# Kernel optimization log

Hardware: AMD Instinct MI355X
Metric: run time of the kernel (lower is better)

The kernel has to match this reference:

```python
import jax, jax.numpy as jnp
import numpy as np

T, B, D = 4096, 8, 256  # tgt_len, batch, embed dim
P, O = 256, 256         # proj_dim, out_dim


def setup_inputs() -> dict:
    key = jax.random.key(0)
    k1, k2, k3, k4, k5 = jax.random.split(key, 5)
    return {
        "query": jax.random.normal(k1, (T, B, D), dtype=jnp.float32),
        "W_kqv": jax.random.normal(k2, (D, 3 * P), dtype=jnp.float32) * (D ** -0.5),
        "b_kqv": jax.random.normal(k3, (3 * P,), dtype=jnp.float32) * 0.02,
        "W_out": jax.random.normal(k4, (P, O), dtype=jnp.float32) * (P ** -0.5),
        "b_out": jax.random.normal(k5, (O,), dtype=jnp.float32) * 0.02,
    }


def reference(query, W_kqv, b_kqv, W_out, b_out):
    # query: [T, B, D] (Time x Batch x Channel)
    p = W_kqv.shape[1] // 3
    scaling = p ** -0.5
    qkv = query @ W_kqv + b_kqv                      # [T, B, 3P]
    q, k, v = jnp.split(qkv, 3, axis=-1)             # each [T, B, P]
    q = (q * scaling).transpose(1, 0, 2)             # [B, T, P]
    k = k.transpose(1, 0, 2)                         # [B, S, P] (S == T)
    v = v.transpose(1, 0, 2)                         # [B, S, P]
    scores = jnp.einsum('btp,bsp->bts', q, k)        # [B, T, S]
    probs = jax.nn.softmax(scores.astype(jnp.float32), axis=-1).astype(q.dtype)
    attn = jnp.einsum('bts,bsp->btp', probs, v)      # [B, T, P]
    attn = attn.transpose(1, 0, 2)                   # [T, B, P]
    return attn @ W_out + b_out                      # [T, B, O]
```

## Files before the change

### kernel.cpp

```cpp
#include <hip/hip_runtime.h>
#include <hip/hip_bf16.h>

#define T_LEN 4096
#define BATCH 8
#define D_DIM 256
#define P_DIM 256
#define O_DIM 256
#define N3    768

typedef __bf16 bf16;
typedef __attribute__((ext_vector_type(8))) __bf16 bf16x8;
typedef __attribute__((ext_vector_type(4))) __bf16 bf16x4;
typedef __attribute__((ext_vector_type(4))) float f32x4;
typedef __attribute__((ext_vector_type(16))) float f32x16;

#define MFMA16(a, b, c) __builtin_amdgcn_mfma_f32_16x16x32_bf16(a, b, c, 0, 0, 0)
#define MFMA32(a, b, c) __builtin_amdgcn_mfma_f32_32x32x16_bf16(a, b, c, 0, 0, 0)

#define LDS_P 72

#define BARRIER_LGKM() __asm__ __volatile__("s_waitcnt lgkmcnt(0)\n\ts_barrier" ::: "memory")

__global__ __launch_bounds__(256) void wpack_kernel(
    const float* __restrict__ src, bf16* __restrict__ dst, int ncols)
{
    const int g = blockIdx.x * 256 + threadIdx.x;
    const int lane = g & 63;
    const int idx = g >> 6;
    const int nt = idx & 3, kt = (idx >> 2) & 7, ch = idx >> 5;
    const int n = ch * 64 + nt * 16 + (lane & 15);
    const int kb = kt * 32 + (lane >> 4) * 8;
    bf16x8 pk;
    #pragma unroll
    for (int j = 0; j < 8; ++j) pk[j] = (bf16)src[(size_t)(kb + j) * ncols + n];
    *(bf16x8*)&dst[(size_t)g * 8] = pk;
}

__global__ __launch_bounds__(256) void qkv_proj_kernel(
    const float* __restrict__ query, const bf16* __restrict__ wkp,
    const float* __restrict__ b_kqv,
    bf16* __restrict__ qb, bf16* __restrict__ kpk, bf16* __restrict__ vpk)
{
    __shared__ __align__(16) bf16 Vt[64][68];
    const int m0 = blockIdx.x * 64;
    const int tid = threadIdx.x;
    const int lane = tid & 63, wave = tid >> 6, l15 = lane & 15, quad = lane >> 4;
    const int arow = wave * 16 + l15;

    bf16x8 af[8];
    {
        const float* qsrc = query + (size_t)(m0 + arow) * D_DIM + quad * 8;
        #pragma unroll
        for (int kt = 0; kt < 8; ++kt) {
            float4 f0 = *(const float4*)(qsrc + kt * 32);
            float4 f1 = *(const float4*)(qsrc + kt * 32 + 4);
            af[kt] = bf16x8{(bf16)f0.x, (bf16)f0.y, (bf16)f0.z, (bf16)f0.w,
                            (bf16)f1.x, (bf16)f1.y, (bf16)f1.z, (bf16)f1.w};
        }
    }

    for (int ch = 0; ch < 12; ++ch) {
        f32x4 acc[4];
        #pragma unroll
        for (int i = 0; i < 4; ++i)
            for (int r = 0; r < 4; ++r) acc[i][r] = 0.f;
        #pragma unroll
        for (int kt = 0; kt < 8; ++kt) {
            #pragma unroll
            for (int nt = 0; nt < 4; ++nt) {
                bf16x8 bb = *(const bf16x8*)&wkp[((((size_t)ch * 8 + kt) * 4 + nt) * 64 + lane) * 8];
                acc[nt] = MFMA16(af[kt], bb, acc[nt]);
            }
        }
        if (ch < 4) {
            #pragma unroll
            for (int nt = 0; nt < 4; ++nt) {
                const int c = ch * 64 + nt * 16 + l15;
                const float bias = b_kqv[c];
                #pragma unroll
                for (int r = 0; r < 4; ++r) {
                    const int m = m0 + wave * 16 + quad * 4 + r;
                    const int t = m >> 3, bi = m & 7;
                    qb[((size_t)bi * T_LEN + t) * P_DIM + c] = (bf16)((acc[nt][r] + bias) * 0.0625f);
                }
            }
        } else if (ch < 8) {
            #pragma unroll
            for (int nt = 0; nt < 4; ++nt) {
                const int c = ch * 64 + nt * 16 + l15;
                const float bias = b_kqv[c];
                const int kk = c - 256;
                const int c16 = kk >> 4, halfk = (kk >> 3) & 1, j = kk & 7;
                #pragma unroll
                for (int r = 0; r < 4; ++r) {
                    const int m = m0 + wave * 16 + quad * 4 + r;
                    const int t = m >> 3, bi = m & 7;
                    const int st32 = t >> 5, n31 = t & 31;
                    kpk[((((size_t)bi * 128 + st32) * 16 + c16) * 64 + halfk * 32 + n31) * 8 + j]
                        = (bf16)(acc[nt][r] + bias);
                }
            }
        } else {
            __syncthreads();
            #pragma unroll
            for (int nt = 0; nt < 4; ++nt) {
                const int c = ch * 64 + nt * 16 + l15;
                const float bias = b_kqv[c];
                #pragma unroll
                for (int r = 0; r < 4; ++r)
                    Vt[nt * 16 + l15][wave * 16 + quad * 4 + r] = (bf16)(acc[nt][r] + bias);
            }
            __syncthreads();
            const int t0g = m0 >> 3;
            const int s64 = t0g >> 6, ks = (t0g >> 4) & 3, halfv = (t0g >> 3) & 1;
            #pragma unroll
            for (int uu = 0; uu < 2; ++uu) {
                const int u = tid * 2 + uu;
                const int cl = u >> 3, bi = u & 7;
                bf16x8 pk;
                #pragma unroll
                for (int j = 0; j < 8; ++j) pk[j] = Vt[cl][j * 8 + bi];
                const int cc = (ch - 8) * 64 + cl;
                const int ptG = cc >> 5, n31 = cc & 31;
                *(bf16x8*)&vpk[((((size_t)bi * 64 + s64) * 4 + ks) * 8 + ptG) * 512
                               + (size_t)(halfv * 32 + n31) * 8] = pk;
            }
        }
    }
}

__global__ __launch_bounds__(256, 2) void flash_attn_kernel(
    const bf16* __restrict__ qb, const bf16* __restrict__ kpk,
    const bf16* __restrict__ vpk, bf16* __restrict__ attn)
{
    __shared__ __align__(16) bf16 Ps[2][64][LDS_P];
    __shared__ float l_red[2][64];

    const int bid = blockIdx.x;
    const int b = bid & 7;
    const int t0 = (bid >> 3) * 64;
    const int tid = threadIdx.x;
    const int lane = tid & 63, wave = tid >> 6;
    const int l31 = lane & 31, half = lane >> 5;
    const int rg = wave & 1, sh = wave >> 1;

    bf16x8 qf[16];
    {
        const bf16* qrow = qb + ((size_t)b * T_LEN + t0 + rg * 32 + l31) * P_DIM + half * 8;
        #pragma unroll
        for (int kt = 0; kt < 16; ++kt) qf[kt] = *(const bf16x8*)(qrow + kt * 16);
    }

    f32x16 acc_o[2][2];
    float l_part[16];
    #pragma unroll
    for (int i = 0; i < 16; ++i) {
        acc_o[0][0][i] = 0.f; acc_o[0][1][i] = 0.f;
        acc_o[1][0][i] = 0.f; acc_o[1][1][i] = 0.f;
        l_part[i] = 0.f;
    }

    const bf16* kfb = kpk + (size_t)b * 128 * 16 * 512;
    const bf16* vfb = vpk + (size_t)b * 64 * 4 * 8 * 512;

    bf16x8 kpre[8];
    {
        const bf16* kf0 = kfb + ((size_t)sh * 16 * 64 + lane) * 8;
        #pragma unroll
        for (int c = 0; c < 8; ++c) kpre[c] = *(const bf16x8*)(kf0 + (size_t)c * 512);
    }

    for (int s0 = 0; s0 < T_LEN; s0 += 64) {
        const int buf = (s0 >> 6) & 1;
        const bf16* kf  = kfb + (((size_t)((s0 >> 5) + sh)) * 16 * 64 + lane) * 8;
        const bf16* kfn = kfb + (((size_t)(((s0 + 64) >> 5) + sh)) * 16 * 64 + lane) * 8;

        bf16x8 kc2[8];
        #pragma unroll
        for (int c = 0; c < 8; ++c) kc2[c] = *(const bf16x8*)(kf + (size_t)(8 + c) * 512);

        f32x16 accs;
        #pragma unroll
        for (int i = 0; i < 16; ++i) accs[i] = 0.f;
        #pragma unroll
        for (int c = 0; c < 8; ++c) accs = MFMA32(qf[c], kpre[c], accs);
        #pragma unroll
        for (int c = 0; c < 8; ++c) accs = MFMA32(qf[8 + c], kc2[c], accs);

        const bf16* vf = vfb + (((size_t)(s0 >> 6) * 4) * 8 + wave * 2) * 512 + (size_t)lane * 8;
        bf16x8 bv[8];
        #pragma unroll
        for (int ks = 0; ks < 4; ++ks) {
            bv[ks * 2]     = *(const bf16x8*)(vf + (size_t)ks * 8 * 512);
            bv[ks * 2 + 1] = *(const bf16x8*)(vf + (size_t)(ks * 8 + 1) * 512);
        }
        #pragma unroll
        for (int c = 0; c < 8; ++c) kpre[c] = *(const bf16x8*)(kfn + (size_t)c * 512);

        #pragma unroll
        for (int r = 0; r < 16; ++r) {
            float p = __expf(accs[r]);
            bf16 pb = (bf16)p;
            l_part[r] += (float)pb;
            int row = rg * 32 + (r & 3) + 8 * (r >> 2) + 4 * half;
            Ps[buf][row][sh * 32 + l31] = pb;
        }

        BARRIER_LGKM();

        #pragma unroll
        for (int ks = 0; ks < 4; ++ks) {
            bf16x8 ap0 = *(const bf16x8*)&Ps[buf][l31][ks * 16 + half * 8];
            bf16x8 ap1 = *(const bf16x8*)&Ps[buf][32 + l31][ks * 16 + half * 8];
            acc_o[0][0] = MFMA32(ap0, bv[ks * 2],     acc_o[0][0]);
            acc_o[0][1] = MFMA32(ap0, bv[ks * 2 + 1], acc_o[0][1]);
            acc_o[1][0] = MFMA32(ap1, bv[ks * 2],     acc_o[1][0]);
            acc_o[1][1] = MFMA32(ap1, bv[ks * 2 + 1], acc_o[1][1]);
        }
    }

    #pragma unroll
    for (int r = 0; r < 16; ++r) {
        float v = l_part[r];
        v += __shfl_xor(v, 1, 64);
        v += __shfl_xor(v, 2, 64);
        v += __shfl_xor(v, 4, 64);
        v += __shfl_xor(v, 8, 64);
        v += __shfl_xor(v, 16, 64);
        l_part[r] = v;
    }
    if (l31 == 0) {
        #pragma unroll
        for (int r = 0; r < 16; ++r) {
            const int row = rg * 32 + (r & 3) + 8 * (r >> 2) + 4 * half;
            l_red[sh][row] = l_part[r];
        }
    }
    __syncthreads();

    #pragma unroll
    for (int rt = 0; rt < 2; ++rt) {
        #pragma unroll
        for (int r = 0; r < 16; ++r) {
            const int row = rt * 32 + (r & 3) + 8 * (r >> 2) + 4 * half;
            const float linv = 1.0f / (l_red[0][row] + l_red[1][row]);
            bf16* dst = attn + ((size_t)(t0 + row) * BATCH + b) * P_DIM + wave * 64 + l31;
            dst[0]  = (bf16)(acc_o[rt][0][r] * linv);
            dst[32] = (bf16)(acc_o[rt][1][r] * linv);
        }
    }
}

__global__ __launch_bounds__(256) void out_proj_kernel(
    const bf16* __restrict__ attn, const bf16* __restrict__ wop,
    const float* __restrict__ b_out, float* __restrict__ out)
{
    const int m0 = blockIdx.x * 64;
    const int tid = threadIdx.x;
    const int lane = tid & 63, wave = tid >> 6, l15 = lane & 15, quad = lane >> 4;
    const int arow = wave * 16 + l15;

    bf16x8 af[8];
    {
        const bf16* asrc = attn + (size_t)(m0 + arow) * P_DIM + quad * 8;
        #pragma unroll
        for (int kt = 0; kt < 8; ++kt) af[kt] = *(const bf16x8*)(asrc + kt * 32);
    }

    for (int ch = 0; ch < 4; ++ch) {
        f32x4 acc[4];
        #pragma unroll
        for (int i = 0; i < 4; ++i)
            for (int r = 0; r < 4; ++r) acc[i][r] = 0.f;
        #pragma unroll
        for (int kt = 0; kt < 8; ++kt) {
            #pragma unroll
            for (int nt = 0; nt < 4; ++nt) {
                bf16x8 bb = *(const bf16x8*)&wop[((((size_t)ch * 8 + kt) * 4 + nt) * 64 + lane) * 8];
                acc[nt] = MFMA16(af[kt], bb, acc[nt]);
            }
        }
        #pragma unroll
        for (int nt = 0; nt < 4; ++nt) {
            const int n = ch * 64 + nt * 16 + l15;
            const float bias = b_out[n];
            #pragma unroll
            for (int r = 0; r < 4; ++r) {
                const int m = m0 + wave * 16 + quad * 4 + r;
                out[(size_t)m * O_DIM + n] = acc[nt][r] + bias;
            }
        }
    }
}

extern "C" void kernel_launch(void* const* d_in, const int* in_sizes, int n_in,
                              void* d_out, int out_size, void* d_ws, size_t ws_size,
                              hipStream_t stream) {
    const float* query = (const float*)d_in[0];
    const float* W_kqv = (const float*)d_in[1];
    const float* b_kqv = (const float*)d_in[2];
    const float* W_out = (const float*)d_in[3];
    const float* b_out = (const float*)d_in[4];
    float* out = (float*)d_out;

    const size_t BUF = (size_t)BATCH * T_LEN * P_DIM;
    bf16* qb   = (bf16*)d_ws;
    bf16* kpk  = qb + BUF;
    bf16* vpk  = kpk + BUF;
    bf16* attn = vpk + BUF;
    bf16* wkp = attn;
    bf16* wop = qb;

    wpack_kernel<<<96, 256, 0, stream>>>(W_kqv, wkp, N3);
    qkv_proj_kernel<<<512, 256, 0, stream>>>(query, wkp, b_kqv, qb, kpk, vpk);
    flash_attn_kernel<<<512, 256, 0, stream>>>(qb, kpk, vpk, attn);
    wpack_kernel<<<32, 256, 0, stream>>>(W_out, wop, O_DIM);
    out_proj_kernel<<<512, 256, 0, stream>>>(attn, wop, b_out, out);
}
```

Before: 283.5 us.

## Software-pipeline attention loop so PV of previous tile overlaps QK of current

Restructures the flash-attention main loop into a two-stage software pipeline. Each iteration computes QK^T and softmax for the current 64-key tile while issuing the PV MFMAs for the previous tile from the other LDS buffer. V fragments are double-buffered in registers (bvA/bvB), and there is a prologue and epilogue. This aims to hide the exp and LDS write latency behind MFMA work and to drop one barrier wait from the critical path, at the cost of more register pressure.

```diff
diff --git a/kernel.cpp b/kernel.cpp
--- a/kernel.cpp
+++ b/kernel.cpp
@@ -170,54 +170,75 @@
         for (int c = 0; c < 8; ++c) kpre[c] = *(const bf16x8*)(kf0 + (size_t)c * 512);
     }
 
-    for (int s0 = 0; s0 < T_LEN; s0 += 64) {
-        const int buf = (s0 >> 6) & 1;
-        const bf16* kf  = kfb + (((size_t)((s0 >> 5) + sh)) * 16 * 64 + lane) * 8;
-        const bf16* kfn = kfb + (((size_t)(((s0 + 64) >> 5) + sh)) * 16 * 64 + lane) * 8;
-
-        bf16x8 kc2[8];
-        #pragma unroll
-        for (int c = 0; c < 8; ++c) kc2[c] = *(const bf16x8*)(kf + (size_t)(8 + c) * 512);
-
-        f32x16 accs;
-        #pragma unroll
-        for (int i = 0; i < 16; ++i) accs[i] = 0.f;
-        #pragma unroll
-        for (int c = 0; c < 8; ++c) accs = MFMA32(qf[c], kpre[c], accs);
-        #pragma unroll
-        for (int c = 0; c < 8; ++c) accs = MFMA32(qf[8 + c], kc2[c], accs);
-
-        const bf16* vf = vfb + (((size_t)(s0 >> 6) * 4) * 8 + wave * 2) * 512 + (size_t)lane * 8;
-        bf16x8 bv[8];
+    bf16x8 bvA[8], bvB[8];
+
+#define FA_ITER(S0, BVP, BVC, DO_PV)                                          \
+{                                                                             \
+    const int buf = ((S0) >> 6) & 1;                                          \
+    const bf16* kf  = kfb + (((size_t)(((S0) >> 5) + sh)) * 16 * 64 + lane) * 8;        \
+    const bf16* kfn = kfb + (((size_t)((((S0) + 64) >> 5) + sh)) * 16 * 64 + lane) * 8; \
+    bf16x8 kc2[8];                                                            \
+    _Pragma("unroll")                                                         \
+    for (int c = 0; c < 8; ++c) kc2[c] = *(const bf16x8*)(kf + (size_t)(8 + c) * 512);  \
+    f32x16 accs;                                                              \
+    _Pragma("unroll")                                                         \
+    for (int i = 0; i < 16; ++i) accs[i] = 0.f;                               \
+    _Pragma("unroll")                                                         \
+    for (int c = 0; c < 8; ++c) accs = MFMA32(qf[c], kpre[c], accs);          \
+    _Pragma("unroll")                                                         \
+    for (int c = 0; c < 8; ++c) accs = MFMA32(qf[8 + c], kc2[c], accs);       \
+    _Pragma("unroll")                                                         \
+    for (int c = 0; c < 8; ++c) kpre[c] = *(const bf16x8*)(kfn + (size_t)c * 512);      \
+    if (DO_PV) {                                                              \
+        const int pbuf = buf ^ 1;                                             \
+        _Pragma("unroll")                                                     \
+        for (int ks = 0; ks < 4; ++ks) {                                      \
+            bf16x8 ap0 = *(const bf16x8*)&Ps[pbuf][l31][ks * 16 + half * 8];  \
+            bf16x8 ap1 = *(const bf16x8*)&Ps[pbuf][32 + l31][ks * 16 + half * 8];       \
+            acc_o[0][0] = MFMA32(ap0, BVP[ks * 2],     acc_o[0][0]);          \
+            acc_o[0][1] = MFMA32(ap0, BVP[ks * 2 + 1], acc_o[0][1]);          \
+            acc_o[1][0] = MFMA32(ap1, BVP[ks * 2],     acc_o[1][0]);          \
+            acc_o[1][1] = MFMA32(ap1, BVP[ks * 2 + 1], acc_o[1][1]);          \
+        }                                                                     \
+    }                                                                         \
+    _Pragma("unroll")                                                         \
+    for (int r = 0; r < 16; ++r) {                                            \
+        float p = __expf(accs[r]);                                            \
+        bf16 pb = (bf16)p;                                                    \
+        l_part[r] += (float)pb;                                               \
+        int row = rg * 32 + (r & 3) + 8 * (r >> 2) + 4 * half;                \
+        Ps[buf][row][sh * 32 + l31] = pb;                                     \
+    }                                                                         \
+    const bf16* vf = vfb + (((size_t)((S0) >> 6) * 4) * 8 + wave * 2) * 512 + (size_t)lane * 8; \
+    _Pragma("unroll")                                                         \
+    for (int ks = 0; ks < 4; ++ks) {                                          \
+        BVC[ks * 2]     = *(const bf16x8*)(vf + (size_t)ks * 8 * 512);        \
+        BVC[ks * 2 + 1] = *(const bf16x8*)(vf + (size_t)(ks * 8 + 1) * 512);  \
+    }                                                                         \
+    BARRIER_LGKM();                                                           \
+}
+
+    FA_ITER(0, bvB, bvA, 0)
+
+    for (int s0 = 64; s0 < 4032; s0 += 128) {
+        FA_ITER(s0,      bvA, bvB, 1)
+        FA_ITER(s0 + 64, bvB, bvA, 1)
+    }
+
+    FA_ITER(4032, bvA, bvB, 1)
+
+    {
         #pragma unroll
         for (int ks = 0; ks < 4; ++ks) {
-            bv[ks * 2]     = *(const bf16x8*)(vf + (size_t)ks * 8 * 512);
-            bv[ks * 2 + 1] = *(const bf16x8*)(vf + (size_t)(ks * 8 + 1) * 512);
-        }
-        #pragma unroll
-        for (int c = 0; c < 8; ++c) kpre[c] = *(const bf16x8*)(kfn + (size_t)c * 512);
-
-        #pragma unroll
-        for (int r = 0; r < 16; ++r) {
-            float p = __expf(accs[r]);
-            bf16 pb = (bf16)p;
-            l_part[r] += (float)pb;
-            int row = rg * 32 + (r & 3) + 8 * (r >> 2) + 4 * half;
-            Ps[buf][row][sh * 32 + l31] = pb;
-        }
-
-        BARRIER_LGKM();
-
-        #pragma unroll
-        for (int ks = 0; ks < 4; ++ks) {
-            bf16x8 ap0 = *(const bf16x8*)&Ps[buf][l31][ks * 16 + half * 8];
-            bf16x8 ap1 = *(const bf16x8*)&Ps[buf][32 + l31][ks * 16 + half * 8];
-            acc_o[0][0] = MFMA32(ap0, bv[ks * 2],     acc_o[0][0]);
-            acc_o[0][1] = MFMA32(ap0, bv[ks * 2 + 1], acc_o[0][1]);
-            acc_o[1][0] = MFMA32(ap1, bv[ks * 2],     acc_o[1][0]);
-            acc_o[1][1] = MFMA32(ap1, bv[ks * 2 + 1], acc_o[1][1]);
-        }
-    }
+            bf16x8 ap0 = *(const bf16x8*)&Ps[1][l31][ks * 16 + half * 8];
+            bf16x8 ap1 = *(const bf16x8*)&Ps[1][32 + l31][ks * 16 + half * 8];
+            acc_o[0][0] = MFMA32(ap0, bvB[ks * 2],     acc_o[0][0]);
+            acc_o[0][1] = MFMA32(ap0, bvB[ks * 2 + 1], acc_o[0][1]);
+            acc_o[1][0] = MFMA32(ap1, bvB[ks * 2],     acc_o[1][0]);
+            acc_o[1][1] = MFMA32(ap1, bvB[ks * 2 + 1], acc_o[1][1]);
+        }
+    }
+#undef FA_ITER
 
     #pragma unroll
     for (int r = 0; r < 16; ++r) {
```

After: 290.2 us. 2.4% more time.

## Enlarge flash-attention tile to 128 query rows with 8 waves per block

Applied to the files above, without the earlier changes.

Each flash-attention block now covers 128 query rows using 512 threads (8 waves) instead of 64 rows with 4 waves. The grid halves to 256 blocks. Each wave computes scores for 32 rows by 32 keys and accumulates a 32-column output slice across all 128 rows. This halves the per-block K/V global traffic relative to the query rows handled and cuts V-fragment registers per wave. In exchange, each block needs more LDS, the barrier spans more waves, and 256 blocks may underfill the CUs on MI355X.

```diff
diff --git a/kernel.cpp b/kernel.cpp
--- a/kernel.cpp
+++ b/kernel.cpp
@@ -129,34 +129,34 @@
     }
 }
 
-__global__ __launch_bounds__(256, 2) void flash_attn_kernel(
+__global__ __launch_bounds__(512, 2) void flash_attn_kernel(
     const bf16* __restrict__ qb, const bf16* __restrict__ kpk,
     const bf16* __restrict__ vpk, bf16* __restrict__ attn)
 {
-    __shared__ __align__(16) bf16 Ps[2][64][LDS_P];
-    __shared__ float l_red[2][64];
+    __shared__ __align__(16) bf16 Ps[2][128][LDS_P];
+    __shared__ float l_red[2][128];
 
     const int bid = blockIdx.x;
     const int b = bid & 7;
-    const int t0 = (bid >> 3) * 64;
+    const int t0 = (bid >> 3) * 128;
     const int tid = threadIdx.x;
     const int lane = tid & 63, wave = tid >> 6;
     const int l31 = lane & 31, half = lane >> 5;
-    const int rg = wave & 1, sh = wave >> 1;
+    const int sh = wave & 1, tg = wave >> 1;
 
     bf16x8 qf[16];
     {
-        const bf16* qrow = qb + ((size_t)b * T_LEN + t0 + rg * 32 + l31) * P_DIM + half * 8;
+        const bf16* qrow = qb + ((size_t)b * T_LEN + t0 + tg * 32 + l31) * P_DIM + half * 8;
         #pragma unroll
         for (int kt = 0; kt < 16; ++kt) qf[kt] = *(const bf16x8*)(qrow + kt * 16);
     }
 
-    f32x16 acc_o[2][2];
+    f32x16 acc_o[4];
     float l_part[16];
     #pragma unroll
     for (int i = 0; i < 16; ++i) {
-        acc_o[0][0][i] = 0.f; acc_o[0][1][i] = 0.f;
-        acc_o[1][0][i] = 0.f; acc_o[1][1][i] = 0.f;
+        acc_o[0][i] = 0.f; acc_o[1][i] = 0.f;
+        acc_o[2][i] = 0.f; acc_o[3][i] = 0.f;
         l_part[i] = 0.f;
     }
 
@@ -187,13 +187,12 @@
         #pragma unroll
         for (int c = 0; c < 8; ++c) accs = MFMA32(qf[8 + c], kc2[c], accs);
 
-        const bf16* vf = vfb + (((size_t)(s0 >> 6) * 4) * 8 + wave * 2) * 512 + (size_t)lane * 8;
-        bf16x8 bv[8];
-        #pragma unroll
-        for (int ks = 0; ks < 4; ++ks) {
-            bv[ks * 2]     = *(const bf16x8*)(vf + (size_t)ks * 8 * 512);
-            bv[ks * 2 + 1] = *(const bf16x8*)(vf + (size_t)(ks * 8 + 1) * 512);
-        }
+        const bf16* vf = vfb + (((size_t)(s0 >> 6) * 4) * 8 + wave) * 512 + (size_t)lane * 8;
+        bf16x8 bv[4];
+        #pragma unroll
+        for (int ks = 0; ks < 4; ++ks)
+            bv[ks] = *(const bf16x8*)(vf + (size_t)ks * 8 * 512);
+
         #pragma unroll
         for (int c = 0; c < 8; ++c) kpre[c] = *(const bf16x8*)(kfn + (size_t)c * 512);
 
@@ -202,7 +201,7 @@
             float p = __expf(accs[r]);
             bf16 pb = (bf16)p;
             l_part[r] += (float)pb;
-            int row = rg * 32 + (r & 3) + 8 * (r >> 2) + 4 * half;
+            int row = tg * 32 + (r & 3) + 8 * (r >> 2) + 4 * half;
             Ps[buf][row][sh * 32 + l31] = pb;
         }
 
@@ -210,12 +209,11 @@
 
         #pragma unroll
         for (int ks = 0; ks < 4; ++ks) {
-            bf16x8 ap0 = *(const bf16x8*)&Ps[buf][l31][ks * 16 + half * 8];
-            bf16x8 ap1 = *(const bf16x8*)&Ps[buf][32 + l31][ks * 16 + half * 8];
-            acc_o[0][0] = MFMA32(ap0, bv[ks * 2],     acc_o[0][0]);
-            acc_o[0][1] = MFMA32(ap0, bv[ks * 2 + 1], acc_o[0][1]);
-            acc_o[1][0] = MFMA32(ap1, bv[ks * 2],     acc_o[1][0]);
-            acc_o[1][1] = MFMA32(ap1, bv[ks * 2 + 1], acc_o[1][1]);
+            #pragma unroll
+            for (int rt = 0; rt < 4; ++rt) {
+                bf16x8 ap = *(const bf16x8*)&Ps[buf][rt * 32 + l31][ks * 16 + half * 8];
+                acc_o[rt] = MFMA32(ap, bv[ks], acc_o[rt]);
+            }
         }
     }
 
@@ -232,21 +230,20 @@
     if (l31 == 0) {
         #pragma unroll
         for (int r = 0; r < 16; ++r) {
-            const int row = rg * 32 + (r & 3) + 8 * (r >> 2) + 4 * half;
+            const int row = tg * 32 + (r & 3) + 8 * (r >> 2) + 4 * half;
             l_red[sh][row] = l_part[r];
         }
     }
     __syncthreads();
 
     #pragma unroll
-    for (int rt = 0; rt < 2; ++rt) {
+    for (int rt = 0; rt < 4; ++rt) {
         #pragma unroll
         for (int r = 0; r < 16; ++r) {
             const int row = rt * 32 + (r & 3) + 8 * (r >> 2) + 4 * half;
             const float linv = 1.0f / (l_red[0][row] + l_red[1][row]);
-            bf16* dst = attn + ((size_t)(t0 + row) * BATCH + b) * P_DIM + wave * 64 + l31;
-            dst[0]  = (bf16)(acc_o[rt][0][r] * linv);
-            dst[32] = (bf16)(acc_o[rt][1][r] * linv);
+            attn[((size_t)(t0 + row) * BATCH + b) * P_DIM + wave * 32 + l31]
+                = (bf16)(acc_o[rt][r] * linv);
         }
     }
 }
@@ -313,7 +310,7 @@
 
     wpack_kernel<<<96, 256, 0, stream>>>(W_kqv, wkp, N3);
     qkv_proj_kernel<<<512, 256, 0, stream>>>(query, wkp, b_kqv, qb, kpk, vpk);
-    flash_attn_kernel<<<512, 256, 0, stream>>>(qb, kpk, vpk, attn);
+    flash_attn_kernel<<<256, 512, 0, stream>>>(qb, kpk, vpk, attn);
     wpack_kernel<<<32, 256, 0, stream>>>(W_out, wop, O_DIM);
     out_proj_kernel<<<512, 256, 0, stream>>>(attn, wop, b_out, out);
 }
```

After: 303.4 us. 7.0% more time.

## Fuse output projection into flash attention epilogue and merge weight packing

Applied to the files above, without the earlier changes.

The normalized attention tile is staged in LDS, and the output projection with bias runs inside the flash attention kernel. This removes the global bf16 attention buffer round-trip and the separate out_proj launch. Both weight-pack launches are merged into one kernel, and the packed W_out moves to its own scratch area so it can be built before attention. The cost is roughly 33 KB more LDS per block, which may reduce occupancy of the attention kernel, plus a longer epilogue.

```diff
diff --git a/kernel.cpp b/kernel.cpp
--- a/kernel.cpp
+++ b/kernel.cpp
@@ -21,10 +21,9 @@
 
 #define BARRIER_LGKM() __asm__ __volatile__("s_waitcnt lgkmcnt(0)\n\ts_barrier" ::: "memory")
 
-__global__ __launch_bounds__(256) void wpack_kernel(
-    const float* __restrict__ src, bf16* __restrict__ dst, int ncols)
+__device__ __forceinline__ void wpack_body(
+    const float* __restrict__ src, bf16* __restrict__ dst, int ncols, int g)
 {
-    const int g = blockIdx.x * 256 + threadIdx.x;
     const int lane = g & 63;
     const int idx = g >> 6;
     const int nt = idx & 3, kt = (idx >> 2) & 7, ch = idx >> 5;
@@ -34,6 +33,18 @@
     #pragma unroll
     for (int j = 0; j < 8; ++j) pk[j] = (bf16)src[(size_t)(kb + j) * ncols + n];
     *(bf16x8*)&dst[(size_t)g * 8] = pk;
+}
+
+__global__ __launch_bounds__(256) void wpack_all_kernel(
+    const float* __restrict__ W_kqv, const float* __restrict__ W_out,
+    bf16* __restrict__ wkp, bf16* __restrict__ wop)
+{
+    const int bid = blockIdx.x;
+    if (bid < 96) {
+        wpack_body(W_kqv, wkp, N3, bid * 256 + threadIdx.x);
+    } else {
+        wpack_body(W_out, wop, O_DIM, (bid - 96) * 256 + threadIdx.x);
+    }
 }
 
 __global__ __launch_bounds__(256) void qkv_proj_kernel(
@@ -131,10 +142,12 @@
 
 __global__ __launch_bounds__(256, 2) void flash_attn_kernel(
     const bf16* __restrict__ qb, const bf16* __restrict__ kpk,
-    const bf16* __restrict__ vpk, bf16* __restrict__ attn)
+    const bf16* __restrict__ vpk, const bf16* __restrict__ wop,
+    const float* __restrict__ b_out, float* __restrict__ out)
 {
     __shared__ __align__(16) bf16 Ps[2][64][LDS_P];
     __shared__ float l_red[2][64];
+    __shared__ __align__(16) bf16 At[64][264];
 
     const int bid = blockIdx.x;
     const int b = bid & 7;
@@ -244,50 +257,42 @@
         for (int r = 0; r < 16; ++r) {
             const int row = rt * 32 + (r & 3) + 8 * (r >> 2) + 4 * half;
             const float linv = 1.0f / (l_red[0][row] + l_red[1][row]);
-            bf16* dst = attn + ((size_t)(t0 + row) * BATCH + b) * P_DIM + wave * 64 + l31;
-            dst[0]  = (bf16)(acc_o[rt][0][r] * linv);
-            dst[32] = (bf16)(acc_o[rt][1][r] * linv);
-        }
-    }
-}
-
-__global__ __launch_bounds__(256) void out_proj_kernel(
-    const bf16* __restrict__ attn, const bf16* __restrict__ wop,
-    const float* __restrict__ b_out, float* __restrict__ out)
-{
-    const int m0 = blockIdx.x * 64;
-    const int tid = threadIdx.x;
-    const int lane = tid & 63, wave = tid >> 6, l15 = lane & 15, quad = lane >> 4;
-    const int arow = wave * 16 + l15;
-
-    bf16x8 af[8];
+            At[row][wave * 64 + l31]      = (bf16)(acc_o[rt][0][r] * linv);
+            At[row][wave * 64 + 32 + l31] = (bf16)(acc_o[rt][1][r] * linv);
+        }
+    }
+    __syncthreads();
+
     {
-        const bf16* asrc = attn + (size_t)(m0 + arow) * P_DIM + quad * 8;
-        #pragma unroll
-        for (int kt = 0; kt < 8; ++kt) af[kt] = *(const bf16x8*)(asrc + kt * 32);
-    }
-
-    for (int ch = 0; ch < 4; ++ch) {
-        f32x4 acc[4];
-        #pragma unroll
-        for (int i = 0; i < 4; ++i)
-            for (int r = 0; r < 4; ++r) acc[i][r] = 0.f;
-        #pragma unroll
-        for (int kt = 0; kt < 8; ++kt) {
-            #pragma unroll
-            for (int nt = 0; nt < 4; ++nt) {
-                bf16x8 bb = *(const bf16x8*)&wop[((((size_t)ch * 8 + kt) * 4 + nt) * 64 + lane) * 8];
-                acc[nt] = MFMA16(af[kt], bb, acc[nt]);
-            }
-        }
-        #pragma unroll
-        for (int nt = 0; nt < 4; ++nt) {
-            const int n = ch * 64 + nt * 16 + l15;
-            const float bias = b_out[n];
-            #pragma unroll
-            for (int r = 0; r < 4; ++r) {
-                const int m = m0 + wave * 16 + quad * 4 + r;
-                out[(size_t)m * O_DIM + n] = acc[nt][r] + bias;
+        const int l15 = lane & 15, quad = lane >> 4;
+        const int arow = wave * 16 + l15;
+        bf16x8 af[8];
+        #pragma unroll
+        for (int kt = 0; kt < 8; ++kt)
+            af[kt] = *(const bf16x8*)&At[arow][quad * 8 + kt * 32];
+
+        for (int ch = 0; ch < 4; ++ch) {
+            f32x4 acc[4];
+            #pragma unroll
+            for (int i = 0; i < 4; ++i)
+                for (int r = 0; r < 4; ++r) acc[i][r] = 0.f;
+            #pragma unroll
+            for (int kt = 0; kt < 8; ++kt) {
+                #pragma unroll
+                for (int nt = 0; nt < 4; ++nt) {
+                    bf16x8 bb = *(const bf16x8*)&wop[((((size_t)ch * 8 + kt) * 4 + nt) * 64 + lane) * 8];
+                    acc[nt] = MFMA16(af[kt], bb, acc[nt]);
+                }
+            }
+            #pragma unroll
+            for (int nt = 0; nt < 4; ++nt) {
+                const int n = ch * 64 + nt * 16 + l15;
+                const float bias = b_out[n];
+                #pragma unroll
+                for (int r = 0; r < 4; ++r) {
+                    const int t = t0 + wave * 16 + quad * 4 + r;
+                    out[((size_t)t * BATCH + b) * O_DIM + n] = acc[nt][r] + bias;
+                }
             }
         }
     }
@@ -307,13 +312,11 @@
     bf16* qb   = (bf16*)d_ws;
     bf16* kpk  = qb + BUF;
     bf16* vpk  = kpk + BUF;
-    bf16* attn = vpk + BUF;
-    bf16* wkp = attn;
-    bf16* wop = qb;
-
-    wpack_kernel<<<96, 256, 0, stream>>>(W_kqv, wkp, N3);
+    bf16* scr  = vpk + BUF;
+    bf16* wkp  = scr;
+    bf16* wop  = scr + 262144;
+
+    wpack_all_kernel<<<128, 256, 0, stream>>>(W_kqv, W_out, wkp, wop);
     qkv_proj_kernel<<<512, 256, 0, stream>>>(query, wkp, b_kqv, qb, kpk, vpk);
-    flash_attn_kernel<<<512, 256, 0, stream>>>(qb, kpk, vpk, attn);
-    wpack_kernel<<<32, 256, 0, stream>>>(W_out, wop, O_DIM);
-    out_proj_kernel<<<512, 256, 0, stream>>>(attn, wop, b_out, out);
-}
+    flash_attn_kernel<<<512, 256, 0, stream>>>(qb, kpk, vpk, wop, b_out, out);
+}
```

Measured after the change: 275.9 us. 1.03x faster.
